# Optimization experiments

Hardware: AMD Instinct MI355X
Metric: run time of the kernel (lower is better)

The kernel has to match this reference:

```python
import jax, jax.numpy as jnp
import numpy as np

B, NGT, G, C = 2, 64, 6, 64
NVOX = 100000            # occupied voxels per batch element
STRIDE = 4               # x_conv3 stride
RADIUS = 0.4             # pool radius (meters)
PCR = (0.0, -40.0, -3.0)
VOX = (0.05, 0.05, 0.1)
DZ, DY, DX = 10, 400, 352  # downsampled sparse grid (z, y, x)


def setup_inputs() -> dict:
    key = jax.random.key(0)
    k = jax.random.split(key, 10)
    cx = jax.random.uniform(k[0], (B, NGT, 1), minval=5.0, maxval=65.0)
    cy = jax.random.uniform(k[1], (B, NGT, 1), minval=-35.0, maxval=35.0)
    cz = jax.random.uniform(k[2], (B, NGT, 1), minval=-1.5, maxval=0.5)
    dims = jax.random.uniform(k[3], (B, NGT, 3), minval=1.5, maxval=4.5)
    heading = jax.random.uniform(k[4], (B, NGT, 1), minval=-np.pi, maxval=np.pi)
    label = jax.random.randint(k[5], (B, NGT, 1), 1, 4).astype(jnp.float32)
    gt_boxes = jnp.concatenate([cx, cy, cz, dims, heading, label], -1)

    def make_voxels(kc, kf):
        kz, ky, kx = jax.random.split(kc, 3)
        z = jax.random.randint(kz, (B * NVOX,), 0, DZ)
        y = jax.random.randint(ky, (B * NVOX,), 0, DY)
        x = jax.random.randint(kx, (B * NVOX,), 0, DX)
        b = jnp.repeat(jnp.arange(B), NVOX)
        coords = jnp.stack([b, z, y, x], 1).astype(jnp.int32)  # (N, 4) bzyx
        feats = jax.random.normal(kf, (B * NVOX, C), dtype=jnp.float32)
        return coords, feats

    cd, fd = make_voxels(k[6], k[7])
    cs, fs = make_voxels(k[8], k[9])
    return {"gt_boxes": gt_boxes,
            "voxel_coords_dir": cd, "voxel_feats_dir": fd,
            "voxel_coords_dsr": cs, "voxel_feats_dsr": fs}


def _grid_points(gt_boxes):
    # get_dense_grid_points + rotate_points_along_z + global shift
    rois = gt_boxes.reshape(-1, gt_boxes.shape[-1])  # (R, 8)
    g = jnp.arange(G, dtype=jnp.float32)
    idx = jnp.stack(jnp.meshgrid(g, g, g, indexing='ij'), -1).reshape(-1, 3)  # (G^3, 3)
    size = rois[:, 3:6]
    local = (idx[None] + 0.5) / G * size[:, None] - size[:, None] * 0.5  # (R, G^3, 3)
    h = rois[:, 6]
    c, s = jnp.cos(h)[:, None], jnp.sin(h)[:, None]
    x, y, z = local[..., 0], local[..., 1], local[..., 2]
    rot = jnp.stack([x * c - y * s, x * s + y * c, z], -1)
    return rot + rois[:, None, 0:3]  # (R, G^3, 3) global grid points


def _pool(grid_xyz, grid_zyx, gbatch, coords, feats):
    # voxel2pinds hash table: (B, DZ, DY, DX) -> point index or -1
    Ntot = coords.shape[0]
    v2p = jnp.full((B, DZ, DY, DX), -1, jnp.int32)
    v2p = v2p.at[coords[:, 0], coords[:, 1], coords[:, 2], coords[:, 3]].set(
        jnp.arange(Ntot, dtype=jnp.int32))
    # voxel centers (get_voxel_centers with downsample=STRIDE)
    vsz = jnp.array([VOX[0] * STRIDE, VOX[1] * STRIDE, VOX[2] * STRIDE], jnp.float32)
    vox_xyz = (coords[:, jnp.array([3, 2, 1])].astype(jnp.float32) + 0.5) * vsz + jnp.array(PCR, jnp.float32)
    # 3x3x3 neighbor window (QUERY_RANGES = [1,1,1])
    o = jnp.arange(-1, 2)
    offs = jnp.stack(jnp.meshgrid(o, o, o, indexing='ij'), -1).reshape(-1, 3)  # (27, 3) zyx
    nb = grid_zyx[:, None, :] + offs[None]  # (M, 27, 3)
    dims = jnp.array([DZ, DY, DX])
    inb = jnp.all((nb >= 0) & (nb < dims), -1)
    nbc = jnp.clip(nb, 0, dims - 1)
    flat = ((gbatch[:, None] * DZ + nbc[..., 0]) * DY + nbc[..., 1]) * DX + nbc[..., 2]
    pidx = v2p.reshape(-1)[flat]  # (M, 27)
    valid = inb & (pidx >= 0)
    psafe = jnp.where(valid, pidx, 0)
    nxyz = vox_xyz[psafe]  # (M, 27, 3)
    d2 = jnp.sum((nxyz - grid_xyz[:, None]) ** 2, -1)
    m = (valid & (d2 < RADIUS * RADIUS)).astype(feats.dtype)  # ball-query mask
    nf = feats[psafe]  # (M, 27, C) irregular gather
    return jnp.einsum('mkc,mk->mc', nf, m) / jnp.maximum(m.sum(-1), 1.0)[:, None]


def _forward(gt_boxes, voxel_coords_dir, voxel_feats_dir, voxel_coords_dsr, voxel_feats_dsr):
    grid = _grid_points(gt_boxes)            # (R, G^3, 3)
    grid_xyz = grid.reshape(-1, 3)           # (M, 3)
    cf = jnp.floor((grid_xyz - jnp.array(PCR, jnp.float32)) / jnp.array(VOX, jnp.float32))
    cds = jnp.floor(cf / STRIDE).astype(jnp.int32)  # xyz coords at stride
    grid_zyx = cds[:, ::-1]
    R = gt_boxes.shape[0] * gt_boxes.shape[1]
    gbatch = jnp.repeat(jnp.arange(B), NGT * G ** 3)

    def branch(coords, feats):
        p = _pool(grid_xyz, grid_zyx, gbatch, coords, feats)  # (M, C)
        gfeat = p.reshape(R, G ** 3, C).mean(1)               # avg_pool1d over grid pts
        n = jnp.sqrt(jnp.sum(gfeat ** 2, -1, keepdims=True))
        return gfeat / jnp.maximum(n, 1e-12)                  # F.normalize(dim=1)

    fdir = branch(voxel_coords_dir, voxel_feats_dir)
    fdsr = branch(voxel_coords_dsr, voxel_feats_dsr)
    return jnp.mean(jnp.abs(jnp.sum(fdir * fdsr, -1)))


def reference(gt_boxes, voxel_coords_dir, voxel_feats_dir, voxel_coords_dsr, voxel_feats_dsr):
    return _forward(gt_boxes, voxel_coords_dir, voxel_feats_dir, voxel_coords_dsr, voxel_feats_dsr)
```

## Files before the change

kernel.cpp:

```cpp
#include <hip/hip_runtime.h>

#define B_     2
#define NGT_   64
#define G_     6
#define C_     64
#define NVOX_  100000
#define DZ_    10
#define DY_    400
#define DX_    352
#define NPTS   (B_ * NVOX_)
#define NROI   (B_ * NGT_)
#define NGP    (G_ * G_ * G_)
#define M_     (NROI * NGP)
#define VCELLS (B_ * DZ_ * DY_ * DX_)

#define WPB    8
#define JPR    (NGP / WPB)
#define PROWS  (M_ / WPB)
#define SCAT_BLOCKS ((2 * NPTS + 255) / 256)
#define POOL_BLOCKS PROWS

__global__ __launch_bounds__(256) void scatter_kernel(
    const int* __restrict__ cdir, const int* __restrict__ cdsr,
    int* __restrict__ v2p, float* __restrict__ out) {
  int i = blockIdx.x * 256 + threadIdx.x;
  if (i == 0) out[0] = 0.0f;
  if (i >= 2 * NPTS) return;
  int br = (i >= NPTS) ? 1 : 0;
  int p  = i - br * NPTS;
  const int* cb = br ? cdsr : cdir;
  int4 v = ((const int4*)cb)[p];
  int flat = ((v.x * DZ_ + v.y) * DY_ + v.z) * DX_ + v.w;
  atomicMax(&v2p[(long long)br * VCELLS + flat], p);
}

__global__ __launch_bounds__(512) void pool_kernel(
    const float* __restrict__ gt,
    const float* __restrict__ fdir, const float* __restrict__ fdsr,
    const int* __restrict__ v2p, float* __restrict__ part) {
#pragma clang fp contract(off)
  __shared__ float red[2][WPB][C_];
  int wid  = threadIdx.x >> 6;
  int lane = threadIdx.x & 63;
  int roi  = blockIdx.x / JPR;
  int j    = blockIdx.x - roi * JPR;
  int gp   = j * WPB + wid;

  const float* r8 = gt + roi * 8;
  float cx = r8[0], cy = r8[1], cz = r8[2];
  float d0 = r8[3], d1 = r8[4], d2s = r8[5];
  float h  = r8[6];

  int ii = gp / 36, jj = (gp / 6) % 6, kk = gp % 6;
  float tx = (ii + 0.5f) / 6.0f;
  float ty = (jj + 0.5f) / 6.0f;
  float tz = (kk + 0.5f) / 6.0f;
  float lx = tx * d0 - d0 * 0.5f;
  float ly = ty * d1 - d1 * 0.5f;
  float lz = tz * d2s - d2s * 0.5f;
  float ch = cosf(h), sh = sinf(h);
  float gx = (lx * ch - ly * sh) + cx;
  float gy = (lx * sh + ly * ch) + cy;
  float gz = lz + cz;

  float fx = floorf((gx - 0.0f)   / 0.05f);
  float fy = floorf((gy + 40.0f)  / 0.05f);
  float fz = floorf((gz + 3.0f)   / 0.1f);
  int ixc = (int)floorf(fx * 0.25f);
  int iyc = (int)floorf(fy * 0.25f);
  int izc = (int)floorf(fz * 0.25f);

  int b = roi >> 6;

  bool geo  = false;
  int  flat = 0;
  if (lane < 27) {
    int oz = lane / 9 - 1, oy = (lane / 3) % 3 - 1, ox = lane % 3 - 1;
    int nz = izc + oz, ny = iyc + oy, nx = ixc + ox;
    if (nz >= 0 && nz < DZ_ && ny >= 0 && ny < DY_ && nx >= 0 && nx < DX_) {
      float vx = ((float)nx + 0.5f) * 0.2f + 0.0f;
      float vy = ((float)ny + 0.5f) * 0.2f + (-40.0f);
      float vz = ((float)nz + 0.5f) * 0.4f + (-3.0f);
      float ddx = vx - gx, ddy = vy - gy, ddz = vz - gz;
      float dd = (ddx * ddx + ddy * ddy) + ddz * ddz;
      if (dd < 0.16f) {
        geo  = true;
        flat = ((b * DZ_ + nz) * DY_ + ny) * DX_ + nx;
      }
    }
  }
  int p0 = -1, p1 = -1;
  if (geo) {
    p0 = v2p[flat];
    p1 = v2p[VCELLS + flat];
  }

  unsigned long long ball0 = __ballot(geo && p0 >= 0);
  unsigned long long ball1 = __ballot(geo && p1 >= 0);
  int cnt0 = __popcll(ball0), cnt1 = __popcll(ball1);
  float acc0 = 0.0f, acc1 = 0.0f;
  unsigned long long m0 = ball0, m1 = ball1;
  while (m0 | m1) {
    int a0 = -1, a1 = -1, a2 = -1, a3 = -1;
    int b0 = -1, b1 = -1, b2 = -1, b3 = -1;
    if (m0) { int k = (int)__builtin_ctzll(m0); m0 &= m0 - 1; a0 = __shfl(p0, k, 64); }
    if (m0) { int k = (int)__builtin_ctzll(m0); m0 &= m0 - 1; a1 = __shfl(p0, k, 64); }
    if (m0) { int k = (int)__builtin_ctzll(m0); m0 &= m0 - 1; a2 = __shfl(p0, k, 64); }
    if (m0) { int k = (int)__builtin_ctzll(m0); m0 &= m0 - 1; a3 = __shfl(p0, k, 64); }
    if (m1) { int k = (int)__builtin_ctzll(m1); m1 &= m1 - 1; b0 = __shfl(p1, k, 64); }
    if (m1) { int k = (int)__builtin_ctzll(m1); m1 &= m1 - 1; b1 = __shfl(p1, k, 64); }
    if (m1) { int k = (int)__builtin_ctzll(m1); m1 &= m1 - 1; b2 = __shfl(p1, k, 64); }
    if (m1) { int k = (int)__builtin_ctzll(m1); m1 &= m1 - 1; b3 = __shfl(p1, k, 64); }
    float va0 = (a0 >= 0) ? fdir[(long long)a0 * C_ + lane] : 0.0f;
    float va1 = (a1 >= 0) ? fdir[(long long)a1 * C_ + lane] : 0.0f;
    float va2 = (a2 >= 0) ? fdir[(long long)a2 * C_ + lane] : 0.0f;
    float va3 = (a3 >= 0) ? fdir[(long long)a3 * C_ + lane] : 0.0f;
    float vb0 = (b0 >= 0) ? fdsr[(long long)b0 * C_ + lane] : 0.0f;
    float vb1 = (b1 >= 0) ? fdsr[(long long)b1 * C_ + lane] : 0.0f;
    float vb2 = (b2 >= 0) ? fdsr[(long long)b2 * C_ + lane] : 0.0f;
    float vb3 = (b3 >= 0) ? fdsr[(long long)b3 * C_ + lane] : 0.0f;
    if (a0 >= 0) acc0 += va0;
    if (a1 >= 0) acc0 += va1;
    if (a2 >= 0) acc0 += va2;
    if (a3 >= 0) acc0 += va3;
    if (b0 >= 0) acc1 += vb0;
    if (b1 >= 0) acc1 += vb1;
    if (b2 >= 0) acc1 += vb2;
    if (b3 >= 0) acc1 += vb3;
  }
  float pooled0 = acc0 / fmaxf((float)cnt0, 1.0f);
  float pooled1 = acc1 / fmaxf((float)cnt1, 1.0f);

  red[0][wid][lane] = pooled0;
  red[1][wid][lane] = pooled1;
  __syncthreads();
  if (wid < 2) {
    float s = 0.0f;
#pragma unroll
    for (int q = 0; q < WPB; ++q) s += red[wid][q][lane];
    part[((long long)wid * PROWS + blockIdx.x) * C_ + lane] = s;
  }
}

__global__ __launch_bounds__(64) void reduce_final_kernel(
    const float* __restrict__ part, float* __restrict__ out) {
  int t = threadIdx.x;
  int r = blockIdx.x;
  const float* pa = part + (long long)r * JPR * C_;
  const float* pb = part + (long long)(PROWS + r * JPR) * C_;
  float a = 0.0f, b = 0.0f;
#pragma unroll
  for (int j = 0; j < JPR; ++j) a += pa[j * C_ + t];
#pragma unroll
  for (int j = 0; j < JPR; ++j) b += pb[j * C_ + t];
  float dot = a * b, na = a * a, nb = b * b;
  for (int off = 32; off; off >>= 1) {
    dot += __shfl_xor(dot, off, 64);
    na  += __shfl_xor(na,  off, 64);
    nb  += __shfl_xor(nb,  off, 64);
  }
  if (t == 0) {
    float term = fabsf(dot) / (fmaxf(sqrtf(na), 1e-12f) * fmaxf(sqrtf(nb), 1e-12f));
    atomicAdd(out, term * (1.0f / 128.0f));
  }
}

extern "C" void kernel_launch(void* const* d_in, const int* in_sizes, int n_in,
                              void* d_out, int out_size, void* d_ws, size_t ws_size,
                              hipStream_t stream) {
  const float* gt   = (const float*)d_in[0];
  const int*   cdir = (const int*)d_in[1];
  const float* fdir = (const float*)d_in[2];
  const int*   cdsr = (const int*)d_in[3];
  const float* fdsr = (const float*)d_in[4];
  float* out = (float*)d_out;

  int*   v2p  = (int*)d_ws;
  float* part = (float*)((char*)d_ws + (size_t)2 * VCELLS * 4);

  scatter_kernel<<<SCAT_BLOCKS, 256, 0, stream>>>(cdir, cdsr, v2p, out);
  pool_kernel<<<POOL_BLOCKS, 512, 0, stream>>>(gt, fdir, fdsr, v2p, part);
  reduce_final_kernel<<<NROI, 64, 0, stream>>>(part, out);
}
```

Before: 151.5 us.

## Fuse scatter, pool and reduce into one cooperative persistent kernel

Merges the three launches (voxel scatter, grid pooling, final reduction) into a single cooperative kernel with a fixed grid of 512 blocks of 512 threads. Grid-wide syncs replace the kernel boundaries, and grid-stride loops cover the scatter and pool work. This removes two launch gaps and the associated tail drain. In exchange it adds grid-sync overhead and caps occupancy at a fixed persistent grid, which may reduce latency hiding in the gather-heavy pool phase.

```diff
diff --git a/kernel.cpp b/kernel.cpp
--- a/kernel.cpp
+++ b/kernel.cpp
@@ -1,4 +1,6 @@
 #include <hip/hip_runtime.h>
+#include <hip/hip_cooperative_groups.h>
+namespace cg = cooperative_groups;
 
 #define B_     2
 #define NGT_   64
@@ -17,151 +19,159 @@
 #define WPB    8
 #define JPR    (NGP / WPB)
 #define PROWS  (M_ / WPB)
-#define SCAT_BLOCKS ((2 * NPTS + 255) / 256)
-#define POOL_BLOCKS PROWS
+#define POOL_UNITS PROWS
 
-__global__ __launch_bounds__(256) void scatter_kernel(
+#define GRID_BLOCKS   512
+#define BLOCK_THREADS 512
+
+__global__ __launch_bounds__(BLOCK_THREADS, 4) void mega_kernel(
+    const float* __restrict__ gt,
     const int* __restrict__ cdir, const int* __restrict__ cdsr,
-    int* __restrict__ v2p, float* __restrict__ out) {
-  int i = blockIdx.x * 256 + threadIdx.x;
-  if (i == 0) out[0] = 0.0f;
-  if (i >= 2 * NPTS) return;
-  int br = (i >= NPTS) ? 1 : 0;
-  int p  = i - br * NPTS;
-  const int* cb = br ? cdsr : cdir;
-  int4 v = ((const int4*)cb)[p];
-  int flat = ((v.x * DZ_ + v.y) * DY_ + v.z) * DX_ + v.w;
-  atomicMax(&v2p[(long long)br * VCELLS + flat], p);
-}
-
-__global__ __launch_bounds__(512) void pool_kernel(
-    const float* __restrict__ gt,
     const float* __restrict__ fdir, const float* __restrict__ fdsr,
-    const int* __restrict__ v2p, float* __restrict__ part) {
+    int* __restrict__ v2p, float* __restrict__ part, float* __restrict__ out) {
 #pragma clang fp contract(off)
   __shared__ float red[2][WPB][C_];
+  cg::grid_group gridg = cg::this_grid();
+  const int tid = blockIdx.x * BLOCK_THREADS + threadIdx.x;
+
+  if (tid == 0) out[0] = 0.0f;
+  for (int i = tid; i < 2 * NPTS; i += GRID_BLOCKS * BLOCK_THREADS) {
+    int br = (i >= NPTS) ? 1 : 0;
+    int p  = i - br * NPTS;
+    const int* cb = br ? cdsr : cdir;
+    int4 v = ((const int4*)cb)[p];
+    int flat = ((v.x * DZ_ + v.y) * DY_ + v.z) * DX_ + v.w;
+    atomicMax(&v2p[(long long)br * VCELLS + flat], p);
+  }
+  gridg.sync();
+
   int wid  = threadIdx.x >> 6;
   int lane = threadIdx.x & 63;
-  int roi  = blockIdx.x / JPR;
-  int j    = blockIdx.x - roi * JPR;
-  int gp   = j * WPB + wid;
+  for (int unit = blockIdx.x; unit < POOL_UNITS; unit += GRID_BLOCKS) {
+    __syncthreads();
+    int roi = unit / JPR;
+    int j   = unit - roi * JPR;
+    int gp  = j * WPB + wid;
 
-  const float* r8 = gt + roi * 8;
-  float cx = r8[0], cy = r8[1], cz = r8[2];
-  float d0 = r8[3], d1 = r8[4], d2s = r8[5];
-  float h  = r8[6];
+    const float* r8 = gt + roi * 8;
+    float cx = r8[0], cy = r8[1], cz = r8[2];
+    float d0 = r8[3], d1 = r8[4], d2s = r8[5];
+    float h  = r8[6];
 
-  int ii = gp / 36, jj = (gp / 6) % 6, kk = gp % 6;
-  float tx = (ii + 0.5f) / 6.0f;
-  float ty = (jj + 0.5f) / 6.0f;
-  float tz = (kk + 0.5f) / 6.0f;
-  float lx = tx * d0 - d0 * 0.5f;
-  float ly = ty * d1 - d1 * 0.5f;
-  float lz = tz * d2s - d2s * 0.5f;
-  float ch = cosf(h), sh = sinf(h);
-  float gx = (lx * ch - ly * sh) + cx;
-  float gy = (lx * sh + ly * ch) + cy;
-  float gz = lz + cz;
+    int ii = gp / 36, jj = (gp / 6) % 6, kk = gp % 6;
+    float tx = (ii + 0.5f) / 6.0f;
+    float ty = (jj + 0.5f) / 6.0f;
+    float tz = (kk + 0.5f) / 6.0f;
+    float lx = tx * d0 - d0 * 0.5f;
+    float ly = ty * d1 - d1 * 0.5f;
+    float lz = tz * d2s - d2s * 0.5f;
+    float ch = cosf(h), sh = sinf(h);
+    float gx = (lx * ch - ly * sh) + cx;
+    float gy = (lx * sh + ly * ch) + cy;
+    float gz = lz + cz;
 
-  float fx = floorf((gx - 0.0f)   / 0.05f);
-  float fy = floorf((gy + 40.0f)  / 0.05f);
-  float fz = floorf((gz + 3.0f)   / 0.1f);
-  int ixc = (int)floorf(fx * 0.25f);
-  int iyc = (int)floorf(fy * 0.25f);
-  int izc = (int)floorf(fz * 0.25f);
+    float fx = floorf((gx - 0.0f)   / 0.05f);
+    float fy = floorf((gy + 40.0f)  / 0.05f);
+    float fz = floorf((gz + 3.0f)   / 0.1f);
+    int ixc = (int)floorf(fx * 0.25f);
+    int iyc = (int)floorf(fy * 0.25f);
+    int izc = (int)floorf(fz * 0.25f);
 
-  int b = roi >> 6;
+    int b = roi >> 6;
 
-  bool geo  = false;
-  int  flat = 0;
-  if (lane < 27) {
-    int oz = lane / 9 - 1, oy = (lane / 3) % 3 - 1, ox = lane % 3 - 1;
-    int nz = izc + oz, ny = iyc + oy, nx = ixc + ox;
-    if (nz >= 0 && nz < DZ_ && ny >= 0 && ny < DY_ && nx >= 0 && nx < DX_) {
-      float vx = ((float)nx + 0.5f) * 0.2f + 0.0f;
-      float vy = ((float)ny + 0.5f) * 0.2f + (-40.0f);
-      float vz = ((float)nz + 0.5f) * 0.4f + (-3.0f);
-      float ddx = vx - gx, ddy = vy - gy, ddz = vz - gz;
-      float dd = (ddx * ddx + ddy * ddy) + ddz * ddz;
-      if (dd < 0.16f) {
-        geo  = true;
-        flat = ((b * DZ_ + nz) * DY_ + ny) * DX_ + nx;
+    bool geo  = false;
+    int  flat = 0;
+    if (lane < 27) {
+      int oz = lane / 9 - 1, oy = (lane / 3) % 3 - 1, ox = lane % 3 - 1;
+      int nz = izc + oz, ny = iyc + oy, nx = ixc + ox;
+      if (nz >= 0 && nz < DZ_ && ny >= 0 && ny < DY_ && nx >= 0 && nx < DX_) {
+        float vx = ((float)nx + 0.5f) * 0.2f + 0.0f;
+        float vy = ((float)ny + 0.5f) * 0.2f + (-40.0f);
+        float vz = ((float)nz + 0.5f) * 0.4f + (-3.0f);
+        float ddx = vx - gx, ddy = vy - gy, ddz = vz - gz;
+        float dd = (ddx * ddx + ddy * ddy) + ddz * ddz;
+        if (dd < 0.16f) {
+          geo  = true;
+          flat = ((b * DZ_ + nz) * DY_ + ny) * DX_ + nx;
+        }
       }
     }
-  }
-  int p0 = -1, p1 = -1;
-  if (geo) {
-    p0 = v2p[flat];
-    p1 = v2p[VCELLS + flat];
+    int p0 = -1, p1 = -1;
+    if (geo) {
+      p0 = v2p[flat];
+      p1 = v2p[VCELLS + flat];
+    }
+
+    unsigned long long ball0 = __ballot(geo && p0 >= 0);
+    unsigned long long ball1 = __ballot(geo && p1 >= 0);
+    int cnt0 = __popcll(ball0), cnt1 = __popcll(ball1);
+    float acc0 = 0.0f, acc1 = 0.0f;
+    unsigned long long m0 = ball0, m1 = ball1;
+    while (m0 | m1) {
+      int a0 = -1, a1 = -1, a2 = -1, a3 = -1;
+      int b0 = -1, b1 = -1, b2 = -1, b3 = -1;
+      if (m0) { int k = (int)__builtin_ctzll(m0); m0 &= m0 - 1; a0 = __shfl(p0, k, 64); }
+      if (m0) { int k = (int)__builtin_ctzll(m0); m0 &= m0 - 1; a1 = __shfl(p0, k, 64); }
+      if (m0) { int k = (int)__builtin_ctzll(m0); m0 &= m0 - 1; a2 = __shfl(p0, k, 64); }
+      if (m0) { int k = (int)__builtin_ctzll(m0); m0 &= m0 - 1; a3 = __shfl(p0, k, 64); }
+      if (m1) { int k = (int)__builtin_ctzll(m1); m1 &= m1 - 1; b0 = __shfl(p1, k, 64); }
+      if (m1) { int k = (int)__builtin_ctzll(m1); m1 &= m1 - 1; b1 = __shfl(p1, k, 64); }
+      if (m1) { int k = (int)__builtin_ctzll(m1); m1 &= m1 - 1; b2 = __shfl(p1, k, 64); }
+      if (m1) { int k = (int)__builtin_ctzll(m1); m1 &= m1 - 1; b3 = __shfl(p1, k, 64); }
+      float va0 = (a0 >= 0) ? fdir[(long long)a0 * C_ + lane] : 0.0f;
+      float va1 = (a1 >= 0) ? fdir[(long long)a1 * C_ + lane] : 0.0f;
+      float va2 = (a2 >= 0) ? fdir[(long long)a2 * C_ + lane] : 0.0f;
+      float va3 = (a3 >= 0) ? fdir[(long long)a3 * C_ + lane] : 0.0f;
+      float vb0 = (b0 >= 0) ? fdsr[(long long)b0 * C_ + lane] : 0.0f;
+      float vb1 = (b1 >= 0) ? fdsr[(long long)b1 * C_ + lane] : 0.0f;
+      float vb2 = (b2 >= 0) ? fdsr[(long long)b2 * C_ + lane] : 0.0f;
+      float vb3 = (b3 >= 0) ? fdsr[(long long)b3 * C_ + lane] : 0.0f;
+      if (a0 >= 0) acc0 += va0;
+      if (a1 >= 0) acc0 += va1;
+      if (a2 >= 0) acc0 += va2;
+      if (a3 >= 0) acc0 += va3;
+      if (b0 >= 0) acc1 += vb0;
+      if (b1 >= 0) acc1 += vb1;
+      if (b2 >= 0) acc1 += vb2;
+      if (b3 >= 0) acc1 += vb3;
+    }
+    float pooled0 = acc0 / fmaxf((float)cnt0, 1.0f);
+    float pooled1 = acc1 / fmaxf((float)cnt1, 1.0f);
+
+    red[0][wid][lane] = pooled0;
+    red[1][wid][lane] = pooled1;
+    __syncthreads();
+    if (wid < 2) {
+      float s = 0.0f;
+#pragma unroll
+      for (int q = 0; q < WPB; ++q) s += red[wid][q][lane];
+      part[((long long)wid * PROWS + unit) * C_ + lane] = s;
+    }
   }
 
-  unsigned long long ball0 = __ballot(geo && p0 >= 0);
-  unsigned long long ball1 = __ballot(geo && p1 >= 0);
-  int cnt0 = __popcll(ball0), cnt1 = __popcll(ball1);
-  float acc0 = 0.0f, acc1 = 0.0f;
-  unsigned long long m0 = ball0, m1 = ball1;
-  while (m0 | m1) {
-    int a0 = -1, a1 = -1, a2 = -1, a3 = -1;
-    int b0 = -1, b1 = -1, b2 = -1, b3 = -1;
-    if (m0) { int k = (int)__builtin_ctzll(m0); m0 &= m0 - 1; a0 = __shfl(p0, k, 64); }
-    if (m0) { int k = (int)__builtin_ctzll(m0); m0 &= m0 - 1; a1 = __shfl(p0, k, 64); }
-    if (m0) { int k = (int)__builtin_ctzll(m0); m0 &= m0 - 1; a2 = __shfl(p0, k, 64); }
-    if (m0) { int k = (int)__builtin_ctzll(m0); m0 &= m0 - 1; a3 = __shfl(p0, k, 64); }
-    if (m1) { int k = (int)__builtin_ctzll(m1); m1 &= m1 - 1; b0 = __shfl(p1, k, 64); }
-    if (m1) { int k = (int)__builtin_ctzll(m1); m1 &= m1 - 1; b1 = __shfl(p1, k, 64); }
-    if (m1) { int k = (int)__builtin_ctzll(m1); m1 &= m1 - 1; b2 = __shfl(p1, k, 64); }
-    if (m1) { int k = (int)__builtin_ctzll(m1); m1 &= m1 - 1; b3 = __shfl(p1, k, 64); }
-    float va0 = (a0 >= 0) ? fdir[(long long)a0 * C_ + lane] : 0.0f;
-    float va1 = (a1 >= 0) ? fdir[(long long)a1 * C_ + lane] : 0.0f;
-    float va2 = (a2 >= 0) ? fdir[(long long)a2 * C_ + lane] : 0.0f;
-    float va3 = (a3 >= 0) ? fdir[(long long)a3 * C_ + lane] : 0.0f;
-    float vb0 = (b0 >= 0) ? fdsr[(long long)b0 * C_ + lane] : 0.0f;
-    float vb1 = (b1 >= 0) ? fdsr[(long long)b1 * C_ + lane] : 0.0f;
-    float vb2 = (b2 >= 0) ? fdsr[(long long)b2 * C_ + lane] : 0.0f;
-    float vb3 = (b3 >= 0) ? fdsr[(long long)b3 * C_ + lane] : 0.0f;
-    if (a0 >= 0) acc0 += va0;
-    if (a1 >= 0) acc0 += va1;
-    if (a2 >= 0) acc0 += va2;
-    if (a3 >= 0) acc0 += va3;
-    if (b0 >= 0) acc1 += vb0;
-    if (b1 >= 0) acc1 += vb1;
-    if (b2 >= 0) acc1 += vb2;
-    if (b3 >= 0) acc1 += vb3;
-  }
-  float pooled0 = acc0 / fmaxf((float)cnt0, 1.0f);
-  float pooled1 = acc1 / fmaxf((float)cnt1, 1.0f);
+  __threadfence();
+  gridg.sync();
 
-  red[0][wid][lane] = pooled0;
-  red[1][wid][lane] = pooled1;
-  __syncthreads();
-  if (wid < 2) {
-    float s = 0.0f;
+  if (blockIdx.x < NROI && threadIdx.x < 64) {
+    int t = threadIdx.x;
+    int r = blockIdx.x;
+    const float* pa = part + (long long)r * JPR * C_;
+    const float* pb = part + (long long)(PROWS + r * JPR) * C_;
+    float a = 0.0f, bsum = 0.0f;
 #pragma unroll
-    for (int q = 0; q < WPB; ++q) s += red[wid][q][lane];
-    part[((long long)wid * PROWS + blockIdx.x) * C_ + lane] = s;
-  }
-}
-
-__global__ __launch_bounds__(64) void reduce_final_kernel(
-    const float* __restrict__ part, float* __restrict__ out) {
-  int t = threadIdx.x;
-  int r = blockIdx.x;
-  const float* pa = part + (long long)r * JPR * C_;
-  const float* pb = part + (long long)(PROWS + r * JPR) * C_;
-  float a = 0.0f, b = 0.0f;
+    for (int jq = 0; jq < JPR; ++jq) a += pa[jq * C_ + t];
 #pragma unroll
-  for (int j = 0; j < JPR; ++j) a += pa[j * C_ + t];
-#pragma unroll
-  for (int j = 0; j < JPR; ++j) b += pb[j * C_ + t];
-  float dot = a * b, na = a * a, nb = b * b;
-  for (int off = 32; off; off >>= 1) {
-    dot += __shfl_xor(dot, off, 64);
-    na  += __shfl_xor(na,  off, 64);
-    nb  += __shfl_xor(nb,  off, 64);
-  }
-  if (t == 0) {
-    float term = fabsf(dot) / (fmaxf(sqrtf(na), 1e-12f) * fmaxf(sqrtf(nb), 1e-12f));
-    atomicAdd(out, term * (1.0f / 128.0f));
+    for (int jq = 0; jq < JPR; ++jq) bsum += pb[jq * C_ + t];
+    float dot = a * bsum, na = a * a, nb = bsum * bsum;
+    for (int off = 32; off; off >>= 1) {
+      dot += __shfl_xor(dot, off, 64);
+      na  += __shfl_xor(na,  off, 64);
+      nb  += __shfl_xor(nb,  off, 64);
+    }
+    if (t == 0) {
+      float term = fabsf(dot) / (fmaxf(sqrtf(na), 1e-12f) * fmaxf(sqrtf(nb), 1e-12f));
+      atomicAdd(out, term * (1.0f / 128.0f));
+    }
   }
 }
 
@@ -178,7 +188,8 @@
   int*   v2p  = (int*)d_ws;
   float* part = (float*)((char*)d_ws + (size_t)2 * VCELLS * 4);
 
-  scatter_kernel<<<SCAT_BLOCKS, 256, 0, stream>>>(cdir, cdsr, v2p, out);
-  pool_kernel<<<POOL_BLOCKS, 512, 0, stream>>>(gt, fdir, fdsr, v2p, part);
-  reduce_final_kernel<<<NROI, 64, 0, stream>>>(part, out);
+  void* args[] = {(void*)&gt, (void*)&cdir, (void*)&cdsr, (void*)&fdir,
+                  (void*)&fdsr, (void*)&v2p, (void*)&part, (void*)&out};
+  hipLaunchCooperativeKernel((const void*)mega_kernel, dim3(GRID_BLOCKS),
+                             dim3(BLOCK_THREADS), args, 0, stream);
 }
```

After: 333.3 us. +120.0%, slower.
